# Kernel optimization log

Measured on AMD Instinct MI355X. Metric: run time of the kernel, lower is better.

The kernel has to match this reference:

```python
import jax, jax.numpy as jnp
import numpy as np

B, S, D, H = 8, 8192, 256, 256


def setup_inputs() -> dict:
    key = jax.random.key(0)
    ks = jax.random.split(key, 5)
    scale = 1.0 / np.sqrt(D)  # mimic nn.Linear init scale
    return {
        "x": jax.random.normal(ks[0], (B, S, D), dtype=jnp.float32),
        "h0": jnp.zeros((B, 1, H), dtype=jnp.float32),
        "w_h_w": jax.random.normal(ks[1], (H, D), dtype=jnp.float32) * scale,
        "w_h_b": jax.random.normal(ks[2], (H,), dtype=jnp.float32) * scale,
        "w_z_w": jax.random.normal(ks[3], (H, D), dtype=jnp.float32) * scale,
        "w_z_b": jax.random.normal(ks[4], (H,), dtype=jnp.float32) * scale,
    }


def reference(x, h0, w_h_w, w_h_b, w_z_w, w_z_b):
    # Projections over the whole sequence (same math as per-step Linear calls)
    z = jax.nn.sigmoid(jnp.einsum('bsd,hd->bsh', x, w_z_w) + w_z_b)  # [B,S,H]
    h_tilde = jnp.einsum('bsd,hd->bsh', x, w_h_w) + w_h_b            # [B,S,H]

    def step(h_prev, zh):
        z_t, ht_t = zh  # each [B,H]
        h_t = (1.0 - z_t) * h_prev + z_t * ht_t
        return h_t, h_t

    # scan over time axis; carry is [B,H]
    _, hs = jax.lax.scan(step, h0[:, 0],
                         (jnp.swapaxes(z, 0, 1), jnp.swapaxes(h_tilde, 0, 1)))
    return jnp.swapaxes(hs, 0, 1)  # [B,S,H]
```

## Files before the change

### kernel.cpp

```cpp
#include <hip/hip_runtime.h>
#include <math.h>


constexpr int B_ = 8;
constexpr int S_ = 8192;
constexpr int D_ = 256;
constexpr int H_ = 256;
constexpr int M_ = B_ * S_;
constexpr int CHUNKS = 128;
constexpr int CLEN = S_ / CHUNKS;

typedef __attribute__((ext_vector_type(8))) short bf16x8;
typedef __attribute__((ext_vector_type(4))) float f32x4;

__device__ __forceinline__ ushort f2bf(float f) {
  union { float f; uint u; } v; v.f = f;
  const uint r = v.u + 0x7FFFu + ((v.u >> 16) & 1u);
  return (ushort)(r >> 16);
}

__global__ __launch_bounds__(256) void gemm_zh(
    const float* __restrict__ x,
    const float* __restrict__ whw, const float* __restrict__ whb,
    const float* __restrict__ wzw, const float* __restrict__ wzb,
    uint* __restrict__ ab)
{
  __shared__ ushort xs[128][72];
  __shared__ ushort wzs[64][72];
  __shared__ ushort whs[64][72];

  const int tid = threadIdx.x;
  const int g    = blockIdx.x;
  const int xcd  = g & 7;
  const int loc  = g >> 3;
  const int nt   = loc & 3;
  const int panel = (loc >> 2) * 8 + xcd;
  const int m0 = panel * 128;
  const int n0 = nt * 64;

  const int lane = tid & 63;
  const int w  = tid >> 6;
  const int mb = (w & 1) * 64;
  const int nb = (w >> 1) * 32;
  const int q  = lane >> 4;
  const int cn = lane & 15;

  f32x4 accz[4][2] = {};
  f32x4 acch[4][2] = {};

  for (int k0 = 0; k0 < D_; k0 += 64) {
    __syncthreads();
#pragma unroll
    for (int f = 0; f < 8; f++) {
      const int idx = tid + 256 * f;
      const int row = idx >> 4, seg = idx & 15;
      float4 v = *(const float4*)(x + (size_t)(m0 + row) * D_ + k0 + seg * 4);
      *(ushort4*)&xs[row][seg * 4] =
          make_ushort4(f2bf(v.x), f2bf(v.y), f2bf(v.z), f2bf(v.w));
    }
#pragma unroll
    for (int f = 0; f < 4; f++) {
      const int idx = tid + 256 * f;
      const int row = idx >> 4, seg = idx & 15;
      float4 vz = *(const float4*)(wzw + (size_t)(n0 + row) * D_ + k0 + seg * 4);
      float4 vh = *(const float4*)(whw + (size_t)(n0 + row) * D_ + k0 + seg * 4);
      *(ushort4*)&wzs[row][seg * 4] =
          make_ushort4(f2bf(vz.x), f2bf(vz.y), f2bf(vz.z), f2bf(vz.w));
      *(ushort4*)&whs[row][seg * 4] =
          make_ushort4(f2bf(vh.x), f2bf(vh.y), f2bf(vh.z), f2bf(vh.w));
    }
    __syncthreads();
#pragma unroll
    for (int ks = 0; ks < 2; ks++) {
      const int kk = ks * 32 + q * 8;
      bf16x8 af[4], bz[2], bh[2];
#pragma unroll
      for (int i = 0; i < 4; i++)
        af[i] = *(const bf16x8*)&xs[mb + i * 16 + cn][kk];
#pragma unroll
      for (int j = 0; j < 2; j++) {
        bz[j] = *(const bf16x8*)&wzs[nb + j * 16 + cn][kk];
        bh[j] = *(const bf16x8*)&whs[nb + j * 16 + cn][kk];
      }
#pragma unroll
      for (int i = 0; i < 4; i++)
#pragma unroll
        for (int j = 0; j < 2; j++) {
          accz[i][j] = __builtin_amdgcn_mfma_f32_16x16x32_bf16(af[i], bz[j], accz[i][j], 0, 0, 0);
          acch[i][j] = __builtin_amdgcn_mfma_f32_16x16x32_bf16(af[i], bh[j], acch[i][j], 0, 0, 0);
        }
    }
  }

#pragma unroll
  for (int j = 0; j < 2; j++) {
    const int ch = n0 + nb + j * 16 + cn;
    const float zb = wzb[ch], hb = whb[ch];
#pragma unroll
    for (int i = 0; i < 4; i++) {
#pragma unroll
      for (int r = 0; r < 4; r++) {
        const int row = m0 + mb + i * 16 + q * 4 + r;
        const float zpre = accz[i][j][r] + zb;
        const float hpre = acch[i][j][r] + hb;
        const float zs = 1.0f / (1.0f + __expf(-zpre));
        const ushort ua = f2bf(1.0f - zs);
        const ushort ub = f2bf(zs * hpre);
        ab[(size_t)row * H_ + ch] = ((uint)ub << 16) | (uint)ua;
      }
    }
  }
}

__global__ __launch_bounds__(256) void scan_phaseA(
    const uint* __restrict__ ab,
    float* __restrict__ P_out, float* __restrict__ Q_out)
{
  const int half = threadIdx.x >> 7;
  const int lt   = threadIdx.x & 127;
  const int c = blockIdx.x * 2 + half;
  const int b = blockIdx.y;
  const int ch = lt * 2;
  size_t base = ((size_t)b * S_ + (size_t)c * CLEN) * H_ + ch;
  float P0 = 1.f, P1 = 1.f, Q0 = 0.f, Q1 = 0.f;
  for (int t0 = 0; t0 < CLEN; t0 += 8) {
    uint2 v[8];
#pragma unroll
    for (int j = 0; j < 8; j++)
      v[j] = *(const uint2*)(ab + base + (size_t)(t0 + j) * H_);
#pragma unroll
    for (int j = 0; j < 8; j++) {
      const float a0 = __uint_as_float(v[j].x << 16);
      const float b0 = __uint_as_float(v[j].x & 0xFFFF0000u);
      const float a1 = __uint_as_float(v[j].y << 16);
      const float b1 = __uint_as_float(v[j].y & 0xFFFF0000u);
      Q0 = fmaf(a0, Q0, b0); P0 *= a0;
      Q1 = fmaf(a1, Q1, b1); P1 *= a1;
    }
  }
  const size_t idx = ((size_t)b * CHUNKS + c) * H_ + ch;
  *(float2*)(P_out + idx) = make_float2(P0, P1);
  *(float2*)(Q_out + idx) = make_float2(Q0, Q1);
}

__global__ __launch_bounds__(256) void scan_phaseB(
    const float* __restrict__ h0in, const float* __restrict__ P,
    const float* __restrict__ Q, float* __restrict__ hstate)
{
  const int b = blockIdx.x;
  const int h = threadIdx.x;
  float hc = h0in[(size_t)b * H_ + h];
  for (int c = 0; c < CHUNKS; c++) {
    const size_t idx = ((size_t)b * CHUNKS + c) * H_ + h;
    hstate[idx] = hc;
    hc = fmaf(P[idx], hc, Q[idx]);
  }
}

__global__ __launch_bounds__(256) void scan_phaseC(
    const uint* __restrict__ ab, const float* __restrict__ hstate,
    float* __restrict__ out)
{
  const int half = threadIdx.x >> 7;
  const int lt   = threadIdx.x & 127;
  const int c = blockIdx.x * 2 + half;
  const int b = blockIdx.y;
  const int ch = lt * 2;
  size_t base = ((size_t)b * S_ + (size_t)c * CLEN) * H_ + ch;
  float2 h = *(const float2*)(hstate + ((size_t)b * CHUNKS + c) * H_ + ch);
  for (int t0 = 0; t0 < CLEN; t0 += 8) {
    uint2 v[8];
#pragma unroll
    for (int j = 0; j < 8; j++)
      v[j] = *(const uint2*)(ab + base + (size_t)(t0 + j) * H_);
#pragma unroll
    for (int j = 0; j < 8; j++) {
      const float a0 = __uint_as_float(v[j].x << 16);
      const float b0 = __uint_as_float(v[j].x & 0xFFFF0000u);
      const float a1 = __uint_as_float(v[j].y << 16);
      const float b1 = __uint_as_float(v[j].y & 0xFFFF0000u);
      h.x = fmaf(a0, h.x, b0);
      h.y = fmaf(a1, h.y, b1);
      *(float2*)(out + base + (size_t)(t0 + j) * H_) = h;
    }
  }
}

extern "C" void kernel_launch(void* const* d_in, const int* in_sizes, int n_in,
                              void* d_out, int out_size, void* d_ws, size_t ws_size,
                              hipStream_t stream) {
  const float* x   = (const float*)d_in[0];
  const float* h0  = (const float*)d_in[1];
  const float* whw = (const float*)d_in[2];
  const float* whb = (const float*)d_in[3];
  const float* wzw = (const float*)d_in[4];
  const float* wzb = (const float*)d_in[5];
  float* out = (float*)d_out;

  uint*  ab     = (uint*)d_ws;
  float* chunkP = (float*)(ab + (size_t)M_ * H_);
  float* chunkQ = chunkP + (size_t)B_ * CHUNKS * H_;
  float* hstate = chunkQ + (size_t)B_ * CHUNKS * H_;

  gemm_zh<<<(M_ / 128) * 4, 256, 0, stream>>>(x, whw, whb, wzw, wzb, ab);
  scan_phaseA<<<dim3(CHUNKS / 2, B_), 256, 0, stream>>>(ab, chunkP, chunkQ);
  scan_phaseB<<<B_, 256, 0, stream>>>(h0, chunkP, chunkQ, hstate);
  scan_phaseC<<<dim3(CHUNKS / 2, B_), 256, 0, stream>>>(ab, hstate, out);
}
```

Before: 197.8 us.

## Fuse chunk-local scan reduction into GEMM epilogue via shared-memory transpose

The GEMM epilogue now stages each block's packed (a,b) tile in shared memory and computes the per-chunk P/Q products directly. This removes the separate phase-A kernel and its full re-read of the ab buffer. The bf16 conversion switches from round-to-nearest-even to a cheaper add-and-permute (round half away), which slightly changes rounding. Phase B now batches its loads, and phase C uses 128-bit accesses with a flattened grid. In exchange, the fused epilogue leaves half the threads idle during the serial 64-step LDS loop.

```diff
diff --git a/kernel.cpp b/kernel.cpp
--- a/kernel.cpp
+++ b/kernel.cpp
@@ -13,21 +13,29 @@
 typedef __attribute__((ext_vector_type(8))) short bf16x8;
 typedef __attribute__((ext_vector_type(4))) float f32x4;
 
-__device__ __forceinline__ ushort f2bf(float f) {
-  union { float f; uint u; } v; v.f = f;
-  const uint r = v.u + 0x7FFFu + ((v.u >> 16) & 1u);
-  return (ushort)(r >> 16);
-}
+__device__ __forceinline__ uint pack2bf(float f0, float f1) {
+  const uint u0 = __float_as_uint(f0) + 0x8000u;
+  const uint u1 = __float_as_uint(f1) + 0x8000u;
+  return __builtin_amdgcn_perm(u1, u0, 0x07060302u);
+}
+
+union SMem {
+  struct {
+    ushort xs[128][72];
+    ushort wzs[64][72];
+    ushort whs[64][72];
+  } s;
+  uint abt[128][66];
+};
 
 __global__ __launch_bounds__(256) void gemm_zh(
     const float* __restrict__ x,
     const float* __restrict__ whw, const float* __restrict__ whb,
     const float* __restrict__ wzw, const float* __restrict__ wzb,
-    uint* __restrict__ ab)
+    uint* __restrict__ ab,
+    float* __restrict__ P_out, float* __restrict__ Q_out)
 {
-  __shared__ ushort xs[128][72];
-  __shared__ ushort wzs[64][72];
-  __shared__ ushort whs[64][72];
+  __shared__ SMem sm;
 
   const int tid = threadIdx.x;
   const int g    = blockIdx.x;
@@ -55,8 +63,8 @@
       const int idx = tid + 256 * f;
       const int row = idx >> 4, seg = idx & 15;
       float4 v = *(const float4*)(x + (size_t)(m0 + row) * D_ + k0 + seg * 4);
-      *(ushort4*)&xs[row][seg * 4] =
-          make_ushort4(f2bf(v.x), f2bf(v.y), f2bf(v.z), f2bf(v.w));
+      *(uint2*)&sm.s.xs[row][seg * 4] =
+          make_uint2(pack2bf(v.x, v.y), pack2bf(v.z, v.w));
     }
 #pragma unroll
     for (int f = 0; f < 4; f++) {
@@ -64,10 +72,10 @@
       const int row = idx >> 4, seg = idx & 15;
       float4 vz = *(const float4*)(wzw + (size_t)(n0 + row) * D_ + k0 + seg * 4);
       float4 vh = *(const float4*)(whw + (size_t)(n0 + row) * D_ + k0 + seg * 4);
-      *(ushort4*)&wzs[row][seg * 4] =
-          make_ushort4(f2bf(vz.x), f2bf(vz.y), f2bf(vz.z), f2bf(vz.w));
-      *(ushort4*)&whs[row][seg * 4] =
-          make_ushort4(f2bf(vh.x), f2bf(vh.y), f2bf(vh.z), f2bf(vh.w));
+      *(uint2*)&sm.s.wzs[row][seg * 4] =
+          make_uint2(pack2bf(vz.x, vz.y), pack2bf(vz.z, vz.w));
+      *(uint2*)&sm.s.whs[row][seg * 4] =
+          make_uint2(pack2bf(vh.x, vh.y), pack2bf(vh.z, vh.w));
     }
     __syncthreads();
 #pragma unroll
@@ -76,11 +84,11 @@
       bf16x8 af[4], bz[2], bh[2];
 #pragma unroll
       for (int i = 0; i < 4; i++)
-        af[i] = *(const bf16x8*)&xs[mb + i * 16 + cn][kk];
+        af[i] = *(const bf16x8*)&sm.s.xs[mb + i * 16 + cn][kk];
 #pragma unroll
       for (int j = 0; j < 2; j++) {
-        bz[j] = *(const bf16x8*)&wzs[nb + j * 16 + cn][kk];
-        bh[j] = *(const bf16x8*)&whs[nb + j * 16 + cn][kk];
+        bz[j] = *(const bf16x8*)&sm.s.wzs[nb + j * 16 + cn][kk];
+        bh[j] = *(const bf16x8*)&sm.s.whs[nb + j * 16 + cn][kk];
       }
 #pragma unroll
       for (int i = 0; i < 4; i++)
@@ -92,55 +100,48 @@
     }
   }
 
+  __syncthreads();
+
 #pragma unroll
   for (int j = 0; j < 2; j++) {
-    const int ch = n0 + nb + j * 16 + cn;
+    const int chl = nb + j * 16 + cn;
+    const int ch = n0 + chl;
     const float zb = wzb[ch], hb = whb[ch];
 #pragma unroll
     for (int i = 0; i < 4; i++) {
 #pragma unroll
       for (int r = 0; r < 4; r++) {
-        const int row = m0 + mb + i * 16 + q * 4 + r;
+        const int rowl = mb + i * 16 + q * 4 + r;
         const float zpre = accz[i][j][r] + zb;
         const float hpre = acch[i][j][r] + hb;
         const float zs = 1.0f / (1.0f + __expf(-zpre));
-        const ushort ua = f2bf(1.0f - zs);
-        const ushort ub = f2bf(zs * hpre);
-        ab[(size_t)row * H_ + ch] = ((uint)ub << 16) | (uint)ua;
+        const uint packed = pack2bf(1.0f - zs, zs * hpre);
+        ab[(size_t)(m0 + rowl) * H_ + ch] = packed;
+        sm.abt[rowl][chl] = packed;
       }
     }
   }
-}
-
-__global__ __launch_bounds__(256) void scan_phaseA(
-    const uint* __restrict__ ab,
-    float* __restrict__ P_out, float* __restrict__ Q_out)
-{
-  const int half = threadIdx.x >> 7;
-  const int lt   = threadIdx.x & 127;
-  const int c = blockIdx.x * 2 + half;
-  const int b = blockIdx.y;
-  const int ch = lt * 2;
-  size_t base = ((size_t)b * S_ + (size_t)c * CLEN) * H_ + ch;
-  float P0 = 1.f, P1 = 1.f, Q0 = 0.f, Q1 = 0.f;
-  for (int t0 = 0; t0 < CLEN; t0 += 8) {
-    uint2 v[8];
-#pragma unroll
-    for (int j = 0; j < 8; j++)
-      v[j] = *(const uint2*)(ab + base + (size_t)(t0 + j) * H_);
-#pragma unroll
-    for (int j = 0; j < 8; j++) {
-      const float a0 = __uint_as_float(v[j].x << 16);
-      const float b0 = __uint_as_float(v[j].x & 0xFFFF0000u);
-      const float a1 = __uint_as_float(v[j].y << 16);
-      const float b1 = __uint_as_float(v[j].y & 0xFFFF0000u);
-      Q0 = fmaf(a0, Q0, b0); P0 *= a0;
-      Q1 = fmaf(a1, Q1, b1); P1 *= a1;
-    }
-  }
-  const size_t idx = ((size_t)b * CHUNKS + c) * H_ + ch;
-  *(float2*)(P_out + idx) = make_float2(P0, P1);
-  *(float2*)(Q_out + idx) = make_float2(Q0, Q1);
+
+  __syncthreads();
+
+  if (tid < 128) {
+    const int k = tid >> 6;
+    const int chl = tid & 63;
+    float P = 1.0f, Q = 0.0f;
+#pragma unroll 8
+    for (int t = 0; t < CLEN; t++) {
+      const uint v = sm.abt[k * 64 + t][chl];
+      const float a = __uint_as_float(v << 16);
+      const float b = __uint_as_float(v & 0xFFFF0000u);
+      Q = fmaf(a, Q, b);
+      P *= a;
+    }
+    const int bidx = m0 / S_;
+    const int cglob = (m0 % S_) / CLEN + k;
+    const size_t idx = ((size_t)bidx * CHUNKS + cglob) * H_ + n0 + chl;
+    P_out[idx] = P;
+    Q_out[idx] = Q;
+  }
 }
 
 __global__ __launch_bounds__(256) void scan_phaseB(
@@ -149,11 +150,20 @@
 {
   const int b = blockIdx.x;
   const int h = threadIdx.x;
+  const size_t base = (size_t)b * CHUNKS * H_ + h;
   float hc = h0in[(size_t)b * H_ + h];
-  for (int c = 0; c < CHUNKS; c++) {
-    const size_t idx = ((size_t)b * CHUNKS + c) * H_ + h;
-    hstate[idx] = hc;
-    hc = fmaf(P[idx], hc, Q[idx]);
+  for (int c0 = 0; c0 < CHUNKS; c0 += 8) {
+    float p[8], q[8];
+#pragma unroll
+    for (int j = 0; j < 8; j++) {
+      p[j] = P[base + (size_t)(c0 + j) * H_];
+      q[j] = Q[base + (size_t)(c0 + j) * H_];
+    }
+#pragma unroll
+    for (int j = 0; j < 8; j++) {
+      hstate[base + (size_t)(c0 + j) * H_] = hc;
+      hc = fmaf(p[j], hc, q[j]);
+    }
   }
 }
 
@@ -161,27 +171,24 @@
     const uint* __restrict__ ab, const float* __restrict__ hstate,
     float* __restrict__ out)
 {
-  const int half = threadIdx.x >> 7;
-  const int lt   = threadIdx.x & 127;
-  const int c = blockIdx.x * 2 + half;
-  const int b = blockIdx.y;
-  const int ch = lt * 2;
-  size_t base = ((size_t)b * S_ + (size_t)c * CLEN) * H_ + ch;
-  float2 h = *(const float2*)(hstate + ((size_t)b * CHUNKS + c) * H_ + ch);
+  const int pair = blockIdx.x * 4 + (threadIdx.x >> 6);
+  const int b = pair >> 7;
+  const int c = pair & 127;
+  const int ch = (threadIdx.x & 63) * 4;
+  const size_t base = ((size_t)b * S_ + (size_t)c * CLEN) * H_ + ch;
+  float4 h = *(const float4*)(hstate + ((size_t)b * CHUNKS + c) * H_ + ch);
   for (int t0 = 0; t0 < CLEN; t0 += 8) {
-    uint2 v[8];
+    uint4 v[8];
 #pragma unroll
     for (int j = 0; j < 8; j++)
-      v[j] = *(const uint2*)(ab + base + (size_t)(t0 + j) * H_);
+      v[j] = *(const uint4*)(ab + base + (size_t)(t0 + j) * H_);
 #pragma unroll
     for (int j = 0; j < 8; j++) {
-      const float a0 = __uint_as_float(v[j].x << 16);
-      const float b0 = __uint_as_float(v[j].x & 0xFFFF0000u);
-      const float a1 = __uint_as_float(v[j].y << 16);
-      const float b1 = __uint_as_float(v[j].y & 0xFFFF0000u);
-      h.x = fmaf(a0, h.x, b0);
-      h.y = fmaf(a1, h.y, b1);
-      *(float2*)(out + base + (size_t)(t0 + j) * H_) = h;
+      h.x = fmaf(__uint_as_float(v[j].x << 16), h.x, __uint_as_float(v[j].x & 0xFFFF0000u));
+      h.y = fmaf(__uint_as_float(v[j].y << 16), h.y, __uint_as_float(v[j].y & 0xFFFF0000u));
+      h.z = fmaf(__uint_as_float(v[j].z << 16), h.z, __uint_as_float(v[j].z & 0xFFFF0000u));
+      h.w = fmaf(__uint_as_float(v[j].w << 16), h.w, __uint_as_float(v[j].w & 0xFFFF0000u));
+      *(float4*)(out + base + (size_t)(t0 + j) * H_) = h;
     }
   }
 }
@@ -202,8 +209,8 @@
   float* chunkQ = chunkP + (size_t)B_ * CHUNKS * H_;
   float* hstate = chunkQ + (size_t)B_ * CHUNKS * H_;
 
-  gemm_zh<<<(M_ / 128) * 4, 256, 0, stream>>>(x, whw, whb, wzw, wzb, ab);
-  scan_phaseA<<<dim3(CHUNKS / 2, B_), 256, 0, stream>>>(ab, chunkP, chunkQ);
+  gemm_zh<<<(M_ / 128) * 4, 256, 0, stream>>>(x, whw, whb, wzw, wzb,
+                                              ab, chunkP, chunkQ);
   scan_phaseB<<<B_, 256, 0, stream>>>(h0, chunkP, chunkQ, hstate);
-  scan_phaseC<<<dim3(CHUNKS / 2, B_), 256, 0, stream>>>(ab, hstate, out);
-}
+  scan_phaseC<<<(B_ * CHUNKS) / 4, 256, 0, stream>>>(ab, hstate, out);
+}
```

Result: no change. 196.8 us (-0.5%).
